# Performance work log

Hardware: AMD Instinct MI355X
Metric: run time of the kernel (lower is better)

## Reference

```python
import jax, jax.numpy as jnp
import numpy as np

D_MODEL = 2048
N_HEADS = 16
HEAD_DIM = 128
WINDOW = 512
ROPE_BASE = 10000.0
B, N = 2, 2048
INNER = N_HEADS * HEAD_DIM


def setup_inputs() -> dict:
    key = jax.random.key(0)
    k1, k2, k3 = jax.random.split(key, 3)
    x = jax.random.normal(k1, (B, N, D_MODEL), dtype=jnp.float32)
    # torch nn.Linear stores weight as [out_features, in_features]
    w_qkv = jax.random.normal(k2, (3 * INNER, D_MODEL), dtype=jnp.float32) / np.sqrt(D_MODEL)
    w_o = jax.random.normal(k3, (D_MODEL, INNER), dtype=jnp.float32) / np.sqrt(INNER)
    return {"x": x, "w_qkv": w_qkv, "w_o": w_o}


def _rotate_half(t):
    t1, t2 = jnp.split(t, 2, axis=-1)
    return jnp.concatenate([-t2, t1], axis=-1)


def _rope(q, k, offset=0):
    # q, k: [B, H, N, D]; GPT-NeoX half-split rotary embedding
    D = q.shape[-1]
    inv_freq = 1.0 / (ROPE_BASE ** (jnp.arange(0, D, 2, dtype=jnp.float32) / D))
    pos = jnp.arange(q.shape[2], dtype=jnp.float32) + offset
    ang = pos[:, None] * inv_freq[None, :]                 # [N, D/2]
    cos = jnp.concatenate([jnp.cos(ang), jnp.cos(ang)], axis=-1)  # [N, D]
    sin = jnp.concatenate([jnp.sin(ang), jnp.sin(ang)], axis=-1)
    q_r = q * cos + _rotate_half(q) * sin
    k_r = k * cos + _rotate_half(k) * sin
    return q_r, k_r


def reference(x, w_qkv, w_o):
    Bq, Nq, _ = x.shape
    # QKV projection (no bias)
    qkv = jnp.einsum('bnd,ed->bne', x, w_qkv)              # [B, N, 3*INNER]
    q, k, v = jnp.split(qkv, 3, axis=-1)
    def to_heads(t):
        return t.reshape(Bq, Nq, N_HEADS, HEAD_DIM).transpose(0, 2, 1, 3)  # [B,H,N,D]
    q, k, v = to_heads(q), to_heads(k), to_heads(v)
    q, k = _rope(q, k, offset=0)
    # sliding-window causal mask: valid key j for query i iff (i - WINDOW) < j <= i
    i = jnp.arange(Nq)[:, None]
    j = jnp.arange(Nq)[None, :]
    valid = (j > i - WINDOW) & (j <= i)                    # [N, N]
    scale = 1.0 / np.sqrt(HEAD_DIM)
    scores = jnp.einsum('bhnd,bhkd->bhnk', q, k) * scale   # [B,H,N,N]
    scores = jnp.where(valid[None, None], scores, -jnp.inf)
    att = jax.nn.softmax(scores, axis=-1)
    out = jnp.einsum('bhnk,bhkd->bhnd', att, v)
    out = out.transpose(0, 2, 1, 3).reshape(Bq, Nq, INNER)
    y = jnp.einsum('bni,di->bnd', out, w_o)
    return y
```

## Files before the change

### kernel.cpp

```cpp
#include <hip/hip_runtime.h>
#include <hip/hip_bf16.h>
#include <cstdint>

typedef __bf16 bf16x8 __attribute__((ext_vector_type(8)));
typedef float floatx4 __attribute__((ext_vector_type(4)));

__device__ __forceinline__ void gl2lds16(const void* g, void* l) {
  __builtin_amdgcn_global_load_lds(
      (const __attribute__((address_space(1))) unsigned int*)g,
      (__attribute__((address_space(3))) unsigned int*)(uintptr_t)l,
      16, 0, 0);
}

__global__ __launch_bounds__(256)
void cvt_kernel(const float* __restrict__ in, __hip_bfloat16* __restrict__ out, int n) {
  int i = (blockIdx.x * 256 + threadIdx.x) * 4;
  if (i >= n) return;
  const float4 v = *(const float4*)(in + i);
  out[i + 0] = __float2bfloat16(v.x);
  out[i + 1] = __float2bfloat16(v.y);
  out[i + 2] = __float2bfloat16(v.z);
  out[i + 3] = __float2bfloat16(v.w);
}

__global__ __launch_bounds__(256)
void cvt2_kernel(const float* __restrict__ in0, const float* __restrict__ in1,
                 __hip_bfloat16* __restrict__ out, int n0, int ntot) {
  int i = (blockIdx.x * 256 + threadIdx.x) * 4;
  if (i >= ntot) return;
  const float4 v = (i < n0) ? *(const float4*)(in0 + i)
                            : *(const float4*)(in1 + (i - n0));
  out[i + 0] = __float2bfloat16(v.x);
  out[i + 1] = __float2bfloat16(v.y);
  out[i + 2] = __float2bfloat16(v.z);
  out[i + 3] = __float2bfloat16(v.w);
}

#define MEMFENCE asm volatile("" ::: "memory")

__global__ __launch_bounds__(512, 4)
void gemm_qkvA(const __hip_bfloat16* __restrict__ A,
               const __hip_bfloat16* __restrict__ W,
               __hip_bfloat16* __restrict__ Qr,
               __hip_bfloat16* __restrict__ Kr,
               __hip_bfloat16* __restrict__ Vt)
{
  extern __shared__ __hip_bfloat16 sm[];
  const int tid = threadIdx.x, lane = tid & 63, wave = tid >> 6;
  const int wr = wave >> 1, wc = wave & 1;
  const int idx = blockIdx.y * 16 + blockIdx.x;
  const int swz = (idx & 7) * 96 + (idx >> 3);
  const int m0 = (swz & 15) << 8;
  const int n0 = (swz >> 4) << 7;
  const int lrow = lane & 15, dg = lane >> 4, lq4 = dg * 4;
  const int rslot = (dg ^ ((lrow >> 1) & 3)) * 8;
  const int arow = tid >> 2;
  const int ascol = ((tid & 3) ^ ((tid >> 3) & 3)) * 8;
  const __hip_bfloat16* aS0 = A + (size_t)(m0 + arow) * 2048 + ascol;
  const __hip_bfloat16* aS1 = A + (size_t)(m0 + 128 + arow) * 2048 + ascol;
  const __hip_bfloat16* bS0 = W + (size_t)(n0 + arow) * 2048 + ascol;
  float* invfp = (float*)((char*)sm + 73728);
  if (tid < 64) invfp[tid] = __expf(-(float)tid * 0.14391156831212787f);
  floatx4 acc[4][4] = {};

#define ASTG(TT) do { const int bo_ = ((TT) % 3) * 12288; const int kk_ = (TT) * 32; \
    gl2lds16(aS0 + kk_, &sm[bo_ + tid * 8]);                                   \
    gl2lds16(aS1 + kk_, &sm[bo_ + 4096 + tid * 8]);                            \
    gl2lds16(bS0 + kk_, &sm[bo_ + 8192 + tid * 8]); } while (0)

#define ACOMP(BO) do {                                                         \
    bf16x8 af[4], bfr[4];                                                      \
    _Pragma("unroll")                                                          \
    for (int mt = 0; mt < 4; mt++)                                             \
      af[mt] = *(const bf16x8*)&sm[(BO) + (wr * 64 + mt * 16 + lrow) * 32 + rslot]; \
    _Pragma("unroll")                                                          \
    for (int nt = 0; nt < 4; nt++)                                             \
      bfr[nt] = *(const bf16x8*)&sm[(BO) + 8192 + (wc * 64 + nt * 16 + lrow) * 32 + rslot]; \
    __builtin_amdgcn_s_setprio(1);                                             \
    _Pragma("unroll")                                                          \
    for (int mt = 0; mt < 4; mt++)                                             \
      _Pragma("unroll")                                                        \
      for (int nt = 0; nt < 4; nt++)                                           \
        acc[mt][nt] = __builtin_amdgcn_mfma_f32_16x16x32_bf16(af[mt], bfr[nt], acc[mt][nt], 0, 0, 0); \
    __builtin_amdgcn_s_setprio(0);                                             \
  } while (0)

  ASTG(0); ASTG(1);
  for (int t = 0; t < 63; ++t) {
    MEMFENCE; __builtin_amdgcn_s_waitcnt(0x0073); MEMFENCE;
    __builtin_amdgcn_s_barrier(); MEMFENCE;
    if (t < 62) ASTG(t + 2);
    ACOMP((t % 3) * 12288);
  }
  MEMFENCE; __builtin_amdgcn_s_waitcnt(0x0070); MEMFENCE;
  __builtin_amdgcn_s_barrier(); MEMFENCE;
  ACOMP((63 % 3) * 12288);
#undef ACOMP
#undef ASTG

  const int seg = n0 >> 11;
  const int h = (n0 & 2047) >> 7;
  const int b = m0 >> 11;
  const int seq0 = m0 & 2047;
  __syncthreads();
  if (seg < 2) {
#pragma unroll
    for (int mt = 0; mt < 4; mt++)
#pragma unroll
      for (int nt = 0; nt < 4; nt++)
#pragma unroll
        for (int r = 0; r < 4; r++)
          sm[(wr * 64 + mt * 16 + lq4 + r) * 136 + wc * 64 + nt * 16 + lrow] =
              __float2bfloat16(acc[mt][nt][r]);
  } else {
#pragma unroll
    for (int mt = 0; mt < 4; mt++)
#pragma unroll
      for (int nt = 0; nt < 4; nt++)
#pragma unroll
        for (int r = 0; r < 4; r++)
          sm[(wc * 64 + nt * 16 + lrow) * 264 + wr * 64 + mt * 16 + lq4 + r] =
              __float2bfloat16(acc[mt][nt][r]);
  }
  __syncthreads();
  const float qs = (seg == 0) ? 0.08838834764831845f : 1.0f;
  if (seg < 2) {
    __hip_bfloat16* Out = seg ? Kr : Qr;
#pragma unroll
    for (int it = 0; it < 4; ++it) {
      const int task = tid + it * 512;
      const int row = task >> 3;
      const int g8 = (task & 7) * 8;
      const int seq = seq0 + row;
      const float pos = (float)seq;
      const bf16x8 lo8 = *(const bf16x8*)&sm[row * 136 + g8];
      const bf16x8 hi8 = *(const bf16x8*)&sm[row * 136 + g8 + 64];
      alignas(16) __hip_bfloat16 lo[8], hi[8];
#pragma unroll
      for (int k = 0; k < 8; k++) {
        float sn, cs;
        __sincosf(pos * invfp[g8 + k], &sn, &cs);
        const float a = (float)lo8[k];
        const float bb2 = (float)hi8[k];
        lo[k] = __float2bfloat16((a * cs - bb2 * sn) * qs);
        hi[k] = __float2bfloat16((bb2 * cs + a * sn) * qs);
      }
      const size_t ob = ((size_t)((b * 16 + h) * 2048 + seq)) * 128;
      *(bf16x8*)&Out[ob + g8] = *(const bf16x8*)lo;
      *(bf16x8*)&Out[ob + g8 + 64] = *(const bf16x8*)hi;
    }
  } else {
#pragma unroll
    for (int it = 0; it < 8; ++it) {
      const int task = tid + it * 512;
      const int col = task >> 5;
      const int sg = (task & 31) * 8;
      const bf16x8 v8 = *(const bf16x8*)&sm[col * 264 + sg];
      *(bf16x8*)&Vt[((size_t)((b * 16 + h) * 128 + col)) * 2048 + seq0 + sg] = v8;
    }
  }
}

__global__ __launch_bounds__(512, 2)
void gemm_o256(const __hip_bfloat16* __restrict__ A,
               const __hip_bfloat16* __restrict__ Wo,
               float* __restrict__ C)
{
  extern __shared__ __hip_bfloat16 sm[];
  const int tid = threadIdx.x, lane = tid & 63, wave = tid >> 6;
  const int wr = wave >> 2, wc = wave & 3;
  const int m0 = blockIdx.x << 8, n0 = blockIdx.y << 7;
  const int lrow = lane & 15, dg = lane >> 4, lq4 = dg * 4;
  const int rslot = (dg ^ ((lrow >> 1) & 3)) * 8;
  const int arow = tid >> 2;
  const int ascol = ((tid & 3) ^ ((tid >> 3) & 3)) * 8;
  const __hip_bfloat16* aS0 = A + (size_t)(m0 + arow) * 2048 + ascol;
  const __hip_bfloat16* aS1 = A + (size_t)(m0 + 128 + arow) * 2048 + ascol;
  const __hip_bfloat16* bS0 = Wo + (size_t)(n0 + arow) * 2048 + ascol;
  floatx4 acc[8][2] = {};

#define OSTAGE(TT) do { const int bb_ = (TT) & 3; const int kk_ = (TT) * 32;   \
    gl2lds16(aS0 + kk_, &sm[bb_ * 12288 + tid * 8]);                           \
    gl2lds16(aS1 + kk_, &sm[bb_ * 12288 + 4096 + tid * 8]);                    \
    gl2lds16(bS0 + kk_, &sm[bb_ * 12288 + 8192 + tid * 8]); } while (0)

#define OKSTEP(TT, WIMM, DOSTAGE) do {                                         \
    MEMFENCE; __builtin_amdgcn_s_waitcnt(WIMM); MEMFENCE;                      \
    __builtin_amdgcn_s_barrier(); MEMFENCE;                                    \
    const int bb = (TT) & 3;                                                   \
    if (DOSTAGE) OSTAGE((TT) + 3);                                             \
    bf16x8 af[8], bfr[2];                                                      \
    _Pragma("unroll")                                                          \
    for (int mt = 0; mt < 8; mt++)                                             \
      af[mt] = *(const bf16x8*)&sm[bb * 12288 + (wr * 128 + mt * 16 + lrow) * 32 + rslot]; \
    _Pragma("unroll")                                                          \
    for (int nt = 0; nt < 2; nt++)                                             \
      bfr[nt] = *(const bf16x8*)&sm[bb * 12288 + 8192 + (wc * 32 + nt * 16 + lrow) * 32 + rslot]; \
    __builtin_amdgcn_s_setprio(1);                                             \
    _Pragma("unroll")                                                          \
    for (int mt = 0; mt < 8; mt++)                                             \
      _Pragma("unroll")                                                        \
      for (int nt = 0; nt < 2; nt++)                                           \
        acc[mt][nt] = __builtin_amdgcn_mfma_f32_16x16x32_bf16(af[mt], bfr[nt], acc[mt][nt], 0, 0, 0); \
    __builtin_amdgcn_s_setprio(0);                                             \
  } while (0)

  OSTAGE(0); OSTAGE(1); OSTAGE(2);
  for (int t = 0; t < 61; ++t) OKSTEP(t, 0x0076, true);
  OKSTEP(61, 0x0076, false);
  OKSTEP(62, 0x0073, false);
  OKSTEP(63, 0x0070, false);
#undef OKSTEP
#undef OSTAGE

#pragma unroll
  for (int mt = 0; mt < 8; mt++)
#pragma unroll
    for (int nt = 0; nt < 2; nt++)
#pragma unroll
      for (int r = 0; r < 4; r++)
        C[(size_t)(m0 + wr * 128 + mt * 16 + lq4 + r) * 2048 +
          (n0 + wc * 32 + nt * 16 + lrow)] = acc[mt][nt][r];
}

#define KSTR 136
#define VSTR 72
__global__ __launch_bounds__(512, 4)
void attn_swa(const __hip_bfloat16* __restrict__ Qr, const __hip_bfloat16* __restrict__ Kr,
              const __hip_bfloat16* __restrict__ Vt, __hip_bfloat16* __restrict__ Out)
{
  __shared__ __hip_bfloat16 Ks[64 * KSTR];
  __shared__ __hip_bfloat16 Vs[128 * VSTR];
  __shared__ __hip_bfloat16 Pb[8][16 * VSTR];
  const int qt = blockIdx.x, bh = blockIdx.y;
  const int tid = threadIdx.x, lane = tid & 63, wave = tid >> 6;
  const int lrow = lane & 15, lk = (lane >> 4) * 8, lq4 = (lane >> 4) * 4;
  const int i0 = qt * 128;
  const float NEG_INF = -__builtin_inff();
  const __hip_bfloat16* Qh = Qr + (size_t)bh * 2048 * 128;
  const __hip_bfloat16* Kh = Kr + (size_t)bh * 2048 * 128;
  const __hip_bfloat16* Vh = Vt + (size_t)bh * 128 * 2048;

  const int ck0 = tid, ck1 = tid + 512;
  const int kr0 = ck0 >> 4, kg0 = (ck0 & 15) * 8;
  const int kr1 = ck1 >> 4, kg1 = (ck1 & 15) * 8;
  const int cv0 = tid, cv1 = tid + 512;
  const int vd0 = cv0 >> 3, vc0 = (cv0 & 7) * 8;
  const int vd1 = cv1 >> 3, vc1 = (cv1 & 7) * 8;

  const int iw = i0 + wave * 16 + lrow;
  bf16x8 qf[4];
#pragma unroll
  for (int ks = 0; ks < 4; ks++)
    qf[ks] = *(const bf16x8*)&Qh[(size_t)iw * 128 + ks * 32 + lk];

  floatx4 accO[8] = {};
  float m_i = NEG_INF, l_i = 0.f;
  const int imin = i0 + wave * 16;
  const int lo = i0 - 511;
  const int jt_lo = (lo > 0 ? lo : 0) >> 6;
  const int jt_hi = (i0 + 127) >> 6;

  int j0n = jt_lo * 64;
  int4 rk0 = *(const int4*)&Kh[(size_t)(j0n + kr0) * 128 + kg0];
  int4 rk1 = *(const int4*)&Kh[(size_t)(j0n + kr1) * 128 + kg1];
  int4 rv0 = *(const int4*)&Vh[(size_t)vd0 * 2048 + j0n + vc0];
  int4 rv1 = *(const int4*)&Vh[(size_t)vd1 * 2048 + j0n + vc1];

  for (int jt = jt_lo; jt <= jt_hi; jt++) {
    const int j0 = jt * 64;
    __syncthreads();
    *(int4*)&Ks[kr0 * KSTR + kg0] = rk0;
    *(int4*)&Ks[kr1 * KSTR + kg1] = rk1;
    *(int4*)&Vs[vd0 * VSTR + vc0] = rv0;
    *(int4*)&Vs[vd1 * VSTR + vc1] = rv1;
    if (jt < jt_hi) {
      const int jn = j0 + 64;
      rk0 = *(const int4*)&Kh[(size_t)(jn + kr0) * 128 + kg0];
      rk1 = *(const int4*)&Kh[(size_t)(jn + kr1) * 128 + kg1];
      rv0 = *(const int4*)&Vh[(size_t)vd0 * 2048 + jn + vc0];
      rv1 = *(const int4*)&Vh[(size_t)vd1 * 2048 + jn + vc1];
    }
    asm volatile("" ::: "memory");
    __builtin_amdgcn_s_waitcnt(0xC07F);
    __builtin_amdgcn_s_barrier();
    asm volatile("" ::: "memory");

    floatx4 s[4] = {};
#pragma unroll
    for (int nt = 0; nt < 4; nt++) {
      const int krow = (nt * 16 + lrow) * KSTR;
#pragma unroll
      for (int ks = 0; ks < 4; ks++) {
        const bf16x8 kf = *(const bf16x8*)&Ks[krow + ks * 32 + lk];
        s[nt] = __builtin_amdgcn_mfma_f32_16x16x32_bf16(kf, qf[ks], s[nt], 0, 0, 0);
      }
    }
    const bool full = (j0 + 63 <= imin) && (j0 >= imin + 15 - 511);
    float rmax = NEG_INF;
    if (full) {
#pragma unroll
      for (int nt = 0; nt < 4; nt++)
#pragma unroll
        for (int r = 0; r < 4; r++) rmax = fmaxf(rmax, s[nt][r]);
    } else {
#pragma unroll
      for (int nt = 0; nt < 4; nt++) {
#pragma unroll
        for (int r = 0; r < 4; r++) {
          const int j = j0 + nt * 16 + lq4 + r;
          const float sv = ((j <= iw) && (j > iw - 512)) ? s[nt][r] : NEG_INF;
          s[nt][r] = sv;
          rmax = fmaxf(rmax, sv);
        }
      }
    }
    rmax = fmaxf(rmax, __shfl_xor(rmax, 16));
    rmax = fmaxf(rmax, __shfl_xor(rmax, 32));
    const float mnew = fmaxf(m_i, rmax);
    const float alpha = __expf(fminf(m_i - mnew, 0.f));
    m_i = mnew;
    float rs = 0.f;
    if (full) {
#pragma unroll
      for (int nt = 0; nt < 4; nt++)
#pragma unroll
        for (int r = 0; r < 4; r++) {
          const float p = __expf(s[nt][r] - mnew);
          s[nt][r] = p;
          rs += p;
        }
    } else {
#pragma unroll
      for (int nt = 0; nt < 4; nt++)
#pragma unroll
        for (int r = 0; r < 4; r++) {
          const float sv = s[nt][r];
          const float p = (sv == NEG_INF) ? 0.f : __expf(sv - mnew);
          s[nt][r] = p;
          rs += p;
        }
    }
    rs += __shfl_xor(rs, 16);
    rs += __shfl_xor(rs, 32);
    l_i = l_i * alpha + rs;
#pragma unroll
    for (int dt = 0; dt < 8; dt++) accO[dt] *= alpha;
#pragma unroll
    for (int nt = 0; nt < 4; nt++) {
      alignas(8) __hip_bfloat16 p4[4];
#pragma unroll
      for (int r = 0; r < 4; r++) p4[r] = __float2bfloat16(s[nt][r]);
      *(uint64_t*)&Pb[wave][lrow * VSTR + nt * 16 + lq4] = *(const uint64_t*)p4;
    }
    bf16x8 pf[2];
#pragma unroll
    for (int jf = 0; jf < 2; jf++)
      pf[jf] = *(const bf16x8*)&Pb[wave][lrow * VSTR + jf * 32 + lk];
#pragma unroll
    for (int dt = 0; dt < 8; dt++) {
      const int vrow = (dt * 16 + lrow) * VSTR;
#pragma unroll
      for (int jf = 0; jf < 2; jf++) {
        const bf16x8 vf = *(const bf16x8*)&Vs[vrow + jf * 32 + lk];
        accO[dt] = __builtin_amdgcn_mfma_f32_16x16x32_bf16(vf, pf[jf], accO[dt], 0, 0, 0);
      }
    }
  }
  const int b = bh >> 4, h = bh & 15;
  const float inv_l = 1.0f / l_i;
  const size_t rowb = ((size_t)(b * 2048 + iw)) * 2048 + h * 128;
#pragma unroll
  for (int dt = 0; dt < 8; dt++) {
    alignas(8) __hip_bfloat16 o4[4];
#pragma unroll
    for (int r = 0; r < 4; r++) o4[r] = __float2bfloat16(accO[dt][r] * inv_l);
    *(uint64_t*)&Out[rowb + dt * 16 + lq4] = *(const uint64_t*)o4;
  }
}

extern "C" void kernel_launch(void* const* d_in, const int* in_sizes, int n_in,
                              void* d_out, int out_size, void* d_ws, size_t ws_size,
                              hipStream_t stream)
{
  const float* x = (const float*)d_in[0];
  const float* w_qkv = (const float*)d_in[1];
  const float* w_o = (const float*)d_in[2];
  float* y = (float*)d_out;
  char* ws = (char*)d_ws;

  const size_t SZ_X = 16777216;
  const size_t SZ_WQKV = 25165824;
  const size_t SZ_Q = 16777216;

  __hip_bfloat16* xb = (__hip_bfloat16*)(ws);
  __hip_bfloat16* wqkvb = (__hip_bfloat16*)(ws + SZ_X);
  __hip_bfloat16* Qr = (__hip_bfloat16*)(ws + SZ_X + SZ_WQKV);
  __hip_bfloat16* Kr = (__hip_bfloat16*)(ws + SZ_X + SZ_WQKV + SZ_Q);
  __hip_bfloat16* Vt = (__hip_bfloat16*)(ws + SZ_X + SZ_WQKV + 2 * SZ_Q);

  static bool s_attr_done = false;
  if (!s_attr_done) {
    hipFuncSetAttribute((const void*)gemm_qkvA,
                        hipFuncAttributeMaxDynamicSharedMemorySize, 73984);
    hipFuncSetAttribute((const void*)gemm_o256,
                        hipFuncAttributeMaxDynamicSharedMemorySize, 98304);
    s_attr_done = true;
  }

  cvt2_kernel<<<dim3(20480), dim3(256), 0, stream>>>(x, w_qkv, xb, 8388608, 20971520);
  gemm_qkvA<<<dim3(16, 48), dim3(512), 73984, stream>>>(xb, wqkvb, Qr, Kr, Vt);
  attn_swa<<<dim3(16, 32), dim3(512), 0, stream>>>(Qr, Kr, Vt, xb );
  cvt_kernel<<<dim3(4096), dim3(256), 0, stream>>>(w_o, wqkvb, 4194304);
  gemm_o256<<<dim3(16, 16), dim3(512), 98304, stream>>>(xb, wqkvb, y);
}
```

Baseline: 340.5 us.

## Shrink QKV GEMM LDS to double buffer and two-pass epilogue for occupancy

The QKV projection GEMM drops from a triple-buffered LDS pipeline to a double-buffered one, adding a second barrier per k-step before the next stage is issued into the buffer just consumed. The epilogue is split into two passes of 128 rows each so the staging tile fits in the smaller LDS footprint, cutting dynamic shared memory from about 72 KB to about 48 KB. The aim is to let more workgroups fit per CU (the launch bounds request 4) so more latency is hidden. The cost is less prefetch depth, an extra barrier per iteration that reduces overlap of loads with MFMA work, and two extra syncthreads in the epilogue.

```diff
diff --git a/kernel.cpp b/kernel.cpp
--- a/kernel.cpp
+++ b/kernel.cpp
@@ -39,7 +39,7 @@
 #define MEMFENCE asm volatile("" ::: "memory")
 
 __global__ __launch_bounds__(512, 4)
-void gemm_qkvA(const __hip_bfloat16* __restrict__ A,
+void gemm_qkvB(const __hip_bfloat16* __restrict__ A,
                const __hip_bfloat16* __restrict__ W,
                __hip_bfloat16* __restrict__ Qr,
                __hip_bfloat16* __restrict__ Kr,
@@ -59,16 +59,16 @@
   const __hip_bfloat16* aS0 = A + (size_t)(m0 + arow) * 2048 + ascol;
   const __hip_bfloat16* aS1 = A + (size_t)(m0 + 128 + arow) * 2048 + ascol;
   const __hip_bfloat16* bS0 = W + (size_t)(n0 + arow) * 2048 + ascol;
-  float* invfp = (float*)((char*)sm + 73728);
+  float* invfp = (float*)((char*)sm + 49152);
   if (tid < 64) invfp[tid] = __expf(-(float)tid * 0.14391156831212787f);
   floatx4 acc[4][4] = {};
 
-#define ASTG(TT) do { const int bo_ = ((TT) % 3) * 12288; const int kk_ = (TT) * 32; \
+#define BSTG(TT) do { const int bo_ = ((TT) & 1) * 12288; const int kk_ = (TT) * 32; \
     gl2lds16(aS0 + kk_, &sm[bo_ + tid * 8]);                                   \
     gl2lds16(aS1 + kk_, &sm[bo_ + 4096 + tid * 8]);                            \
     gl2lds16(bS0 + kk_, &sm[bo_ + 8192 + tid * 8]); } while (0)
 
-#define ACOMP(BO) do {                                                         \
+#define BCOMP(BO) do {                                                         \
     bf16x8 af[4], bfr[4];                                                      \
     _Pragma("unroll")                                                          \
     for (int mt = 0; mt < 4; mt++)                                             \
@@ -85,78 +85,86 @@
     __builtin_amdgcn_s_setprio(0);                                             \
   } while (0)
 
-  ASTG(0); ASTG(1);
+  BSTG(0); BSTG(1);
   for (int t = 0; t < 63; ++t) {
     MEMFENCE; __builtin_amdgcn_s_waitcnt(0x0073); MEMFENCE;
     __builtin_amdgcn_s_barrier(); MEMFENCE;
-    if (t < 62) ASTG(t + 2);
-    ACOMP((t % 3) * 12288);
+    BCOMP((t & 1) * 12288);
+    if (t <= 61) {
+      MEMFENCE; __builtin_amdgcn_s_barrier(); MEMFENCE;
+      BSTG(t + 2);
+    }
   }
   MEMFENCE; __builtin_amdgcn_s_waitcnt(0x0070); MEMFENCE;
   __builtin_amdgcn_s_barrier(); MEMFENCE;
-  ACOMP((63 % 3) * 12288);
-#undef ACOMP
-#undef ASTG
+  BCOMP(12288);
+#undef BCOMP
+#undef BSTG
 
   const int seg = n0 >> 11;
   const int h = (n0 & 2047) >> 7;
   const int b = m0 >> 11;
   const int seq0 = m0 & 2047;
-  __syncthreads();
-  if (seg < 2) {
-#pragma unroll
-    for (int mt = 0; mt < 4; mt++)
-#pragma unroll
-      for (int nt = 0; nt < 4; nt++)
-#pragma unroll
-        for (int r = 0; r < 4; r++)
-          sm[(wr * 64 + mt * 16 + lq4 + r) * 136 + wc * 64 + nt * 16 + lrow] =
-              __float2bfloat16(acc[mt][nt][r]);
-  } else {
-#pragma unroll
-    for (int mt = 0; mt < 4; mt++)
-#pragma unroll
-      for (int nt = 0; nt < 4; nt++)
-#pragma unroll
-        for (int r = 0; r < 4; r++)
-          sm[(wc * 64 + nt * 16 + lrow) * 264 + wr * 64 + mt * 16 + lq4 + r] =
-              __float2bfloat16(acc[mt][nt][r]);
-  }
-  __syncthreads();
   const float qs = (seg == 0) ? 0.08838834764831845f : 1.0f;
-  if (seg < 2) {
-    __hip_bfloat16* Out = seg ? Kr : Qr;
-#pragma unroll
-    for (int it = 0; it < 4; ++it) {
-      const int task = tid + it * 512;
-      const int row = task >> 3;
-      const int g8 = (task & 7) * 8;
-      const int seq = seq0 + row;
-      const float pos = (float)seq;
-      const bf16x8 lo8 = *(const bf16x8*)&sm[row * 136 + g8];
-      const bf16x8 hi8 = *(const bf16x8*)&sm[row * 136 + g8 + 64];
-      alignas(16) __hip_bfloat16 lo[8], hi[8];
-#pragma unroll
-      for (int k = 0; k < 8; k++) {
-        float sn, cs;
-        __sincosf(pos * invfp[g8 + k], &sn, &cs);
-        const float a = (float)lo8[k];
-        const float bb2 = (float)hi8[k];
-        lo[k] = __float2bfloat16((a * cs - bb2 * sn) * qs);
-        hi[k] = __float2bfloat16((bb2 * cs + a * sn) * qs);
-      }
-      const size_t ob = ((size_t)((b * 16 + h) * 2048 + seq)) * 128;
-      *(bf16x8*)&Out[ob + g8] = *(const bf16x8*)lo;
-      *(bf16x8*)&Out[ob + g8 + 64] = *(const bf16x8*)hi;
-    }
-  } else {
-#pragma unroll
-    for (int it = 0; it < 8; ++it) {
-      const int task = tid + it * 512;
-      const int col = task >> 5;
-      const int sg = (task & 31) * 8;
-      const bf16x8 v8 = *(const bf16x8*)&sm[col * 264 + sg];
-      *(bf16x8*)&Vt[((size_t)((b * 16 + h) * 128 + col)) * 2048 + seq0 + sg] = v8;
+  for (int p = 0; p < 2; ++p) {
+    __syncthreads();
+    if ((wr >> 1) == p) {
+      const int rb = (wr & 1) * 64;
+      if (seg < 2) {
+#pragma unroll
+        for (int mt = 0; mt < 4; mt++)
+#pragma unroll
+          for (int nt = 0; nt < 4; nt++)
+#pragma unroll
+            for (int r = 0; r < 4; r++)
+              sm[(rb + mt * 16 + lq4 + r) * 136 + wc * 64 + nt * 16 + lrow] =
+                  __float2bfloat16(acc[mt][nt][r]);
+      } else {
+#pragma unroll
+        for (int mt = 0; mt < 4; mt++)
+#pragma unroll
+          for (int nt = 0; nt < 4; nt++)
+#pragma unroll
+            for (int r = 0; r < 4; r++)
+              sm[(wc * 64 + nt * 16 + lrow) * 136 + rb + mt * 16 + lq4 + r] =
+                  __float2bfloat16(acc[mt][nt][r]);
+      }
+    }
+    __syncthreads();
+    if (seg < 2) {
+      __hip_bfloat16* Out = seg ? Kr : Qr;
+#pragma unroll
+      for (int it = 0; it < 2; ++it) {
+        const int task = tid + it * 512;
+        const int row = task >> 3;
+        const int g8 = (task & 7) * 8;
+        const int seq = seq0 + p * 128 + row;
+        const float pos = (float)seq;
+        const bf16x8 lo8 = *(const bf16x8*)&sm[row * 136 + g8];
+        const bf16x8 hi8 = *(const bf16x8*)&sm[row * 136 + g8 + 64];
+        alignas(16) __hip_bfloat16 lo[8], hi[8];
+#pragma unroll
+        for (int k = 0; k < 8; k++) {
+          float sn, cs;
+          __sincosf(pos * invfp[g8 + k], &sn, &cs);
+          const float a = (float)lo8[k];
+          const float bb2 = (float)hi8[k];
+          lo[k] = __float2bfloat16((a * cs - bb2 * sn) * qs);
+          hi[k] = __float2bfloat16((bb2 * cs + a * sn) * qs);
+        }
+        const size_t ob = ((size_t)((b * 16 + h) * 2048 + seq)) * 128;
+        *(bf16x8*)&Out[ob + g8] = *(const bf16x8*)lo;
+        *(bf16x8*)&Out[ob + g8 + 64] = *(const bf16x8*)hi;
+      }
+    } else {
+#pragma unroll
+      for (int it = 0; it < 4; ++it) {
+        const int task = tid + it * 512;
+        const int col = task >> 4;
+        const int sg = (task & 15) * 8;
+        const bf16x8 v8 = *(const bf16x8*)&sm[col * 136 + sg];
+        *(bf16x8*)&Vt[((size_t)((b * 16 + h) * 128 + col)) * 2048 + seq0 + p * 128 + sg] = v8;
+      }
     }
   }
 }
@@ -401,15 +409,15 @@
 
   static bool s_attr_done = false;
   if (!s_attr_done) {
-    hipFuncSetAttribute((const void*)gemm_qkvA,
-                        hipFuncAttributeMaxDynamicSharedMemorySize, 73984);
+    hipFuncSetAttribute((const void*)gemm_qkvB,
+                        hipFuncAttributeMaxDynamicSharedMemorySize, 49408);
     hipFuncSetAttribute((const void*)gemm_o256,
                         hipFuncAttributeMaxDynamicSharedMemorySize, 98304);
     s_attr_done = true;
   }
 
   cvt2_kernel<<<dim3(20480), dim3(256), 0, stream>>>(x, w_qkv, xb, 8388608, 20971520);
-  gemm_qkvA<<<dim3(16, 48), dim3(512), 73984, stream>>>(xb, wqkvb, Qr, Kr, Vt);
+  gemm_qkvB<<<dim3(16, 48), dim3(512), 49408, stream>>>(xb, wqkvb, Qr, Kr, Vt);
   attn_swa<<<dim3(16, 32), dim3(512), 0, stream>>>(Qr, Kr, Vt, xb );
   cvt_kernel<<<dim3(4096), dim3(256), 0, stream>>>(w_o, wqkvb, 4194304);
   gemm_o256<<<dim3(16, 16), dim3(512), 98304, stream>>>(xb, wqkvb, y);
```

New measurement: 345.9 us. No clear change (+1.6%).
